# Optimization experiments

Hardware: AMD Instinct MI355X
Metric: run time of the kernel (lower is better)

The kernel has to match this reference:

```python
import jax, jax.numpy as jnp
import numpy as np

S = 1024   # qlen = klen (mems=None)
B = 4
D = 1024   # d_model
N = 16     # n_head
H = 64     # d_head
R = 2 * S  # relative position embedding length = klen + qlen
EPS = 1e-12
SCALE = float(1.0 / np.sqrt(H))


def setup_inputs() -> dict:
    key = jax.random.key(0)
    ks = jax.random.split(key, 14)
    h = jax.random.normal(ks[0], (S, B, D), dtype=jnp.float32)
    r = jax.random.normal(ks[1], (R, B, D), dtype=jnp.float32)
    # segment ids -> one-hot same/diff segment matrix [i, j, b, 2]
    seg_ids = jax.random.randint(ks[2], (S, B), 0, 2)
    diff = (seg_ids[:, None, :] != seg_ids[None, :, :]).astype(jnp.int32)  # [S,S,B]
    seg_mat = jax.nn.one_hot(diff, 2, dtype=jnp.float32)  # [S,S,B,2]
    # causal attention mask: 1 where key position j > query position i
    causal = (jnp.arange(S)[None, :] > jnp.arange(S)[:, None]).astype(jnp.float32)
    attn_mask = jnp.broadcast_to(causal[:, :, None, None], (S, S, B, 1))
    w = lambda k, shape: 0.02 * jax.random.normal(k, shape, dtype=jnp.float32)
    return {
        "h": h, "r": r, "seg_mat": seg_mat, "attn_mask": attn_mask,
        "Wq": w(ks[3], (D, N, H)), "Wk": w(ks[4], (D, N, H)),
        "Wv": w(ks[5], (D, N, H)), "Wo": w(ks[6], (D, N, H)),
        "Wr": w(ks[7], (D, N, H)),
        "r_w_bias": w(ks[8], (N, H)), "r_r_bias": w(ks[9], (N, H)),
        "r_s_bias": w(ks[10], (N, H)), "seg_embed": w(ks[11], (2, N, H)),
        "ln_scale": jnp.ones((D,), jnp.float32), "ln_bias": jnp.zeros((D,), jnp.float32),
    }


def rel_shift_bnij(x, klen):
    # x: [b, n, i, j_r] with j_r = klen + qlen
    b, n, i, j = x.shape
    x = x.reshape(b, n, j, i)[:, :, 1:, :].reshape(b, n, i, j - 1)
    return x[:, :, :, :klen]


def layer_norm(x, scale, bias):
    mu = jnp.mean(x, axis=-1, keepdims=True)
    var = jnp.mean(jnp.square(x - mu), axis=-1, keepdims=True)
    return (x - mu) * jax.lax.rsqrt(var + EPS) * scale + bias


def reference(h, r, seg_mat, attn_mask, Wq, Wk, Wv, Wo, Wr,
              r_w_bias, r_r_bias, r_s_bias, seg_embed, ln_scale, ln_bias):
    # projections (mems=None => cat = h)
    q_head = jnp.einsum('ibh,hnd->ibnd', h, Wq)
    k_head_h = jnp.einsum('ibh,hnd->ibnd', h, Wk)
    v_head_h = jnp.einsum('ibh,hnd->ibnd', h, Wv)
    k_head_r = jnp.einsum('ibh,hnd->ibnd', r, Wr)

    klen = k_head_h.shape[0]
    # content-based score
    ac = jnp.einsum('ibnd,jbnd->bnij', q_head + r_w_bias, k_head_h)
    # position-based score with relative shift
    bd = jnp.einsum('ibnd,jbnd->bnij', q_head + r_r_bias, k_head_r)
    bd = rel_shift_bnij(bd, klen)
    # segment-based score
    ef = jnp.einsum('ibnd,snd->ibns', q_head + r_s_bias, seg_embed)
    ef = jnp.einsum('ijbs,ibns->bnij', seg_mat, ef)

    attn_score = (ac + bd + ef) * SCALE
    attn_score = attn_score - 1e30 * jnp.transpose(attn_mask, (2, 3, 0, 1))  # ijbn->bnij
    attn_prob = jax.nn.softmax(attn_score, axis=3)

    attn_vec = jnp.einsum('bnij,jbnd->ibnd', attn_prob, v_head_h)
    attn_out = jnp.einsum('ibnd,hnd->ibh', attn_vec, Wo) + h  # residual
    return layer_norm(attn_out, ln_scale, ln_bias)
```

## Files before the change

### kernel.cpp

```cpp
#include <hip/hip_runtime.h>

#define Sq 1024
#define Bb 4
#define Dm 1024
#define Nh 16
#define Hd 64

typedef unsigned short ushort_t;
typedef __attribute__((ext_vector_type(8))) short s8v;
typedef __attribute__((ext_vector_type(8))) unsigned short us8;
typedef __attribute__((ext_vector_type(4))) float f32x4;
typedef __attribute__((ext_vector_type(2))) __fp16 fp16x2;

__device__ __forceinline__ float bf2f(ushort_t u) {
  union { unsigned int i; float f; } t; t.i = ((unsigned int)u) << 16; return t.f;
}
__device__ __forceinline__ ushort_t f2bf(float f) {
  union { float f; unsigned int i; } t; t.f = f;
  unsigned int lsb = (t.i >> 16) & 1u;
  t.i += 0x7fffu + lsb;
  return (ushort_t)(t.i >> 16);
}

__device__ __forceinline__ void load4(const float* p, float* o) {
  const float4 v = *(const float4*)p;
  o[0] = v.x; o[1] = v.y; o[2] = v.z; o[3] = v.w;
}

__device__ __forceinline__ float wave_reduce_sum(float v) {
#pragma unroll
  for (int off = 32; off; off >>= 1) v += __shfl_xor(v, off, 64);
  return v;
}

__device__ __forceinline__ void gl_lds16(const ushort_t* g, ushort_t* l) {
  __builtin_amdgcn_global_load_lds(
      (const __attribute__((address_space(1))) unsigned int*)g,
      (__attribute__((address_space(3))) unsigned int*)l, 16, 0, 0);
}

template <int MODE>
__device__ __forceinline__ void gemm128(const ushort_t* __restrict__ A,
                                        const ushort_t* __restrict__ B,
                                        void* __restrict__ Cv,
                                        const float* __restrict__ bias0,
                                        int bm, int bn) {
  __shared__ ushort_t As[128 * 32];
  __shared__ ushort_t Bs[128 * 32];
  const int tid = threadIdx.x;
  const int w = tid >> 6, lane = tid & 63;
  const int quad = lane >> 4, l16 = lane & 15;
  const int wm = (w & 1) * 64, wn = (w >> 1) * 64;
  const int srow0 = 32 * w + (lane >> 2);
  const int scb = (lane & 3) * 16;
  f32x4 acc[4][4] = {};

  for (int k0 = 0; k0 < 1024; k0 += 32) {
    __syncthreads();
#pragma unroll
    for (int c = 0; c < 2; ++c) {
      const int row = srow0 + c * 16;
      const int cbs = scb ^ (((row >> 1) & 3) << 4);
      gl_lds16(A + (size_t)(bm + row) * 1024 + k0 + (cbs >> 1),
               &As[(32 * w + c * 16) * 32]);
      gl_lds16(B + (size_t)(bn + row) * 1024 + k0 + (cbs >> 1),
               &Bs[(32 * w + c * 16) * 32]);
    }
    __syncthreads();
    s8v av[4], bv[4];
    const int sw = ((l16 >> 1) & 3) << 4;
    const int cbb = ((quad * 16) ^ sw) >> 1;
#pragma unroll
    for (int i = 0; i < 4; ++i) {
      av[i] = *(const s8v*)&As[(wm + i * 16 + l16) * 32 + cbb];
      bv[i] = *(const s8v*)&Bs[(wn + i * 16 + l16) * 32 + cbb];
    }
#pragma unroll
    for (int i = 0; i < 4; ++i)
#pragma unroll
      for (int j = 0; j < 4; ++j)
        acc[i][j] = __builtin_amdgcn_mfma_f32_16x16x32_bf16(av[i], bv[j], acc[i][j], 0, 0, 0);
  }

  float bj[4];
  if (MODE == 3) {
#pragma unroll
    for (int j = 0; j < 4; ++j) bj[j] = bias0[bn + wn + j * 16 + l16];
  }
#pragma unroll
  for (int i = 0; i < 4; ++i) {
#pragma unroll
    for (int j = 0; j < 4; ++j) {
      const int cg = bn + wn + j * 16 + l16;
#pragma unroll
      for (int reg = 0; reg < 4; ++reg) {
        const int mg = bm + wm + i * 16 + quad * 4 + reg;
        const float v = acc[i][j][reg];
        if (MODE == 3) {
          ((ushort_t*)Cv)[((size_t)(cg >> 6) * 1024 + mg) * 64 + (cg & 63)] =
              f2bf((v + bj[j]) * 0.125f);
        } else if (MODE == 0) {
          ((ushort_t*)Cv)[((size_t)(cg >> 6) * 1024 + mg) * 64 + (cg & 63)] = f2bf(v);
        } else {
          ((float*)Cv)[(size_t)mg * 1024 + cg] = v;
        }
      }
    }
  }
}

__global__ __launch_bounds__(256) void conv_hr(const float* __restrict__ h,
                                               const float* __restrict__ r,
                                               const float* __restrict__ Wo,
                                               ushort_t* __restrict__ h_bf,
                                               ushort_t* __restrict__ r_bf,
                                               ushort_t* __restrict__ Wo_bf) {
  const int i = blockIdx.x, b = blockIdx.y;
  const int d0 = threadIdx.x * 4;
  {
    const float4 v = *(const float4*)&h[(size_t)(i * 4 + b) * 1024 + d0];
    ushort4 o; o.x = f2bf(v.x); o.y = f2bf(v.y); o.z = f2bf(v.z); o.w = f2bf(v.w);
    *(ushort4*)&h_bf[(size_t)b * 1048576 + (size_t)i * 1024 + d0] = o;
  }
  {
    const float4 v = *(const float4*)&r[(size_t)(i * 4 + 4 + b) * 1024 + d0];
    ushort4 o; o.x = f2bf(v.x); o.y = f2bf(v.y); o.z = f2bf(v.z); o.w = f2bf(v.w);
    *(ushort4*)&r_bf[(size_t)b * 1048576 + (size_t)i * 1024 + d0] = o;
  }
  if (b == 0) {
    const float4 v = *(const float4*)&Wo[(size_t)i * 1024 + d0];
    ushort4 o; o.x = f2bf(v.x); o.y = f2bf(v.y); o.z = f2bf(v.z); o.w = f2bf(v.w);
    *(ushort4*)&Wo_bf[(size_t)i * 1024 + d0] = o;
  }
}

__global__ __launch_bounds__(256) void conv_wt(const float* __restrict__ Wq,
                                               const float* __restrict__ Wk,
                                               const float* __restrict__ Wv,
                                               const float* __restrict__ Wr,
                                               ushort_t* __restrict__ Wt) {
  const int z = blockIdx.z;
  const float* W = (z == 0) ? Wq : (z == 1) ? Wk : (z == 2) ? Wv : Wr;
  ushort_t* O = Wt + (size_t)z * 1048576;
  __shared__ float t[64][68];
  const int n0 = blockIdx.x * 64, k0 = blockIdx.y * 64;
  const int tr = threadIdx.x >> 4, tc = (threadIdx.x & 15) * 4;
#pragma unroll
  for (int rr = 0; rr < 4; ++rr) {
    const int r_ = tr + rr * 16;
    const float4 v = *(const float4*)&W[(size_t)(k0 + r_) * 1024 + n0 + tc];
    t[r_][tc] = v.x; t[r_][tc + 1] = v.y; t[r_][tc + 2] = v.z; t[r_][tc + 3] = v.w;
  }
  __syncthreads();
#pragma unroll
  for (int rr = 0; rr < 4; ++rr) {
    const int nr = tr + rr * 16;
    ushort4 o;
    o.x = f2bf(t[tc + 0][nr]); o.y = f2bf(t[tc + 1][nr]);
    o.z = f2bf(t[tc + 2][nr]); o.w = f2bf(t[tc + 3][nr]);
    *(ushort4*)&O[(size_t)(n0 + nr) * 1024 + k0 + tc] = o;
  }
}

__global__ __launch_bounds__(256) void sseg_kernel(const float* __restrict__ seg_mat,
                                                   const float* __restrict__ rwb,
                                                   const float* __restrict__ rrb,
                                                   float* __restrict__ sseg,
                                                   float* __restrict__ drr) {
  const int idx = blockIdx.x * 256 + threadIdx.x;
  const int b = idx >> 10, j = idx & 1023;
  sseg[b * 1024 + j] = seg_mat[(size_t)j * 8 + b * 2 + 1];
  if (idx < 1024) drr[idx] = (rrb[idx] - rwb[idx]) * 0.125f;
}

__global__ __launch_bounds__(256) void projA(
    const ushort_t* __restrict__ h_bf, const ushort_t* __restrict__ r_bf,
    const ushort_t* __restrict__ Wt, const float* __restrict__ rwb,
    ushort_t* __restrict__ qcS, ushort_t* __restrict__ KSl,
    ushort_t* __restrict__ KRS) {
  const int z = blockIdx.z, zi = z % 3, b = z / 3;
  const int zz = (zi == 2) ? 3 : zi;
  const size_t slab = (size_t)Nh * Sq * Hd;
  const ushort_t* A = (zz == 3 ? r_bf : h_bf) + (size_t)b * 1048576;
  const ushort_t* B = Wt + (size_t)zz * 1048576;
  const int bm = blockIdx.y * 128, bn = blockIdx.x * 128;
  if (zi == 0) gemm128<3>(A, B, qcS + b * slab, rwb, bm, bn);
  else if (zi == 1) gemm128<0>(A, B, KSl + b * slab, nullptr, bm, bn);
  else gemm128<0>(A, B, KRS + b * slab, nullptr, bm, bn);
}

__global__ __launch_bounds__(256) void projV(const ushort_t* __restrict__ h_bf,
                                             const ushort_t* __restrict__ Wt,
                                             ushort_t* __restrict__ VS) {
  const int b = blockIdx.z;
  const size_t slab = (size_t)Nh * Sq * Hd;
  gemm128<0>(h_bf + (size_t)b * 1048576, Wt + (size_t)2 * 1048576, VS + b * slab,
             nullptr, blockIdx.y * 128, blockIdx.x * 128);
}

__global__ __launch_bounds__(256) void vtrans(const ushort_t* __restrict__ VS,
                                              ushort_t* __restrict__ VTP) {
  const int j0 = blockIdx.x * 64, n = blockIdx.y, b = blockIdx.z;
  const size_t slab = (size_t)Nh * Sq * Hd;
  const ushort_t* src = VS + b * slab + (size_t)n * Sq * Hd;
  ushort_t* dst = VTP + b * slab + (size_t)n * Hd * Sq;
  __shared__ ushort_t t[64][72];
  const int tid = threadIdx.x;
#pragma unroll
  for (int it = 0; it < 2; ++it) {
    const int row = it * 32 + (tid >> 3);
    const int c = (tid & 7) * 8;
    const us8 v = *(const us8*)&src[(size_t)(j0 + row) * 64 + c];
#pragma unroll
    for (int e = 0; e < 8; ++e) t[row][c + e] = v[e];
  }
  __syncthreads();
#pragma unroll
  for (int it = 0; it < 2; ++it) {
    const int idx = it * 256 + tid;
    const int d = idx >> 3;
    const int kc = (idx & 7) * 8;
    us8 o;
#pragma unroll
    for (int e = 0; e < 8; ++e) {
      const int k = kc + e;
      o[e] = t[(k & 3) * 16 + (k >> 2)][d];
    }
    *(us8*)&dst[(size_t)d * Sq + j0 + kc] = o;
  }
}

__global__ __launch_bounds__(256) void attn_mfma(
    const ushort_t* __restrict__ QCS, const ushort_t* __restrict__ KS,
    const ushort_t* __restrict__ VTS, const ushort_t* __restrict__ KRS,
    const float* __restrict__ rwb, const float* __restrict__ rsb,
    const float* __restrict__ seg_embed, const float* __restrict__ sseg,
    const float* __restrict__ drr, ushort_t* __restrict__ AVbf) {
  const int nb = blockIdx.x;
  const int n = nb & 15, b = nb >> 4;
  const int i0b = (int)(gridDim.y - 1 - blockIdx.y) * 32;
  const int tid = threadIdx.x;
  const int w = tid >> 6, lane = tid & 63;
  const int quad = lane >> 4, l16 = lane & 15;
  const int ht = w >> 1;
  const int jp = w & 1;
  const int i0s = i0b + ht * 16;
  const size_t slab = (size_t)Nh * Sq * Hd;
  const size_t nS = (size_t)n * Sq;
  const ushort_t* Qh = QCS + b * slab + nS * Hd;
  const ushort_t* Kh = KS + b * slab + nS * Hd;
  const ushort_t* Vh = VTS + b * slab + (size_t)n * Hd * Sq;
  const ushort_t* KRh = KRS + b * slab + nS * Hd;
  const float* ssegb = sseg + b * Sq;

  __shared__ ushort_t P_s[4][16 * 64];
  __shared__ float o_s[2][2][16][66];
  __shared__ float l_s[2][2][16];

  s8v qc[2], qr[2];
  float efa_v, efb_v;
  {
    const int qrow = i0s + l16;
    const size_t qbase = (size_t)qrow * 64;
    float p0 = 0.f, p1 = 0.f;
#pragma unroll
    for (int ks = 0; ks < 2; ++ks) {
      const int dl = ks * 32 + quad * 8;
      const int db = n * 64 + dl;
      const s8v qv = *(const s8v*)&Qh[qbase + dl];
      qc[ks] = qv;
      float dr8[8], w8[8], s8a[8], e08[8], e18[8];
      load4(drr + db, dr8); load4(drr + db + 4, dr8 + 4);
      load4(rwb + db, w8);  load4(rwb + db + 4, w8 + 4);
      load4(rsb + db, s8a); load4(rsb + db + 4, s8a + 4);
      load4(seg_embed + db, e08); load4(seg_embed + db + 4, e08 + 4);
      load4(seg_embed + Nh * 64 + db, e18); load4(seg_embed + Nh * 64 + db + 4, e18 + 4);
#pragma unroll
      for (int e = 0; e < 8; ++e) {
        const float qcf = bf2f((ushort_t)qv[e]);
        qr[ks][e] = (short)f2bf(qcf + dr8[e]);
        const float qs = qcf * 8.f - w8[e] + s8a[e];
        p0 += qs * e08[e];
        p1 += qs * e18[e];
      }
    }
    p0 += __shfl_xor(p0, 16, 64); p0 += __shfl_xor(p0, 32, 64);
    p1 += __shfl_xor(p1, 16, 64); p1 += __shfl_xor(p1, 32, 64);
    const float si = ssegb[qrow];
    const float de = p1 - p0;
    efa_v = (p0 + de * si) * 0.125f;
    efb_v = de * (1.f - 2.f * si) * 0.125f;
  }

  float efa_r[4], efb_r[4];
  int bp_idx[4], selhi[4];
#pragma unroll
  for (int reg = 0; reg < 4; ++reg) {
    const int il = quad * 4 + reg;
    efa_r[reg] = __shfl(efa_v, il, 64);
    efb_r[reg] = __shfl(efb_v, il, 64);
    const int off = l16 + 15 - il;
    bp_idx[reg] = (((quad << 4) | (off & 15)) << 2);
    selhi[reg] = off >> 4;
  }

  f32x4 o[4] = {};
  float l_r[4] = {0.f, 0.f, 0.f, 0.f};
  char* Pb = (char*)P_s[w];

  const int n_jt = i0s / 64 + 1;
  for (int jt = jp; jt < n_jt; jt += 2) {
    const int j0 = jt * 64;
    const bool last = (jt == n_jt - 1);

    f32x4 sc[4];
    const ushort_t* Kt = Kh + (size_t)j0 * 64;
#pragma unroll
    for (int u = 0; u < 4; ++u) {
      const int ro = (u * 16 + l16) * 64 + quad * 8;
      f32x4 a = {};
      a = __builtin_amdgcn_mfma_f32_16x16x32_bf16(qc[0], *(const s8v*)&Kt[ro], a, 0, 0, 0);
      a = __builtin_amdgcn_mfma_f32_16x16x32_bf16(qc[1], *(const s8v*)&Kt[ro + 32], a, 0, 0, 0);
      sc[u] = a;
    }

    f32x4 bdw[5];
    const ushort_t* KRt = KRh + (size_t)(1008 + j0 - i0s) * 64;
    const int rlim = 15 + (i0s & 63);
#pragma unroll
    for (int u = 0; u < 5; ++u) {
      int rr = u * 16 + l16;
      if (last && rr > rlim) rr = rlim;
      const int ro = rr * 64 + quad * 8;
      f32x4 a = {};
      a = __builtin_amdgcn_mfma_f32_16x16x32_bf16(qr[0], *(const s8v*)&KRt[ro], a, 0, 0, 0);
      a = __builtin_amdgcn_mfma_f32_16x16x32_bf16(qr[1], *(const s8v*)&KRt[ro + 32], a, 0, 0, 0);
      bdw[u] = a;
    }

    int pk[4][4];
#pragma unroll
    for (int u = 0; u < 4; ++u)
#pragma unroll
      for (int reg = 0; reg < 4; ++reg) {
        const fp16x2 t = __builtin_amdgcn_cvt_pkrtz(bdw[u][reg], bdw[u + 1][reg]);
        pk[u][reg] = __builtin_bit_cast(int, t);
      }

    float sj[4];
#pragma unroll
    for (int u = 0; u < 4; ++u) sj[u] = ssegb[j0 + u * 16 + l16];
    float p[4][4];
#pragma unroll
    for (int u = 0; u < 4; ++u) {
#pragma unroll
      for (int reg = 0; reg < 4; ++reg) {
        const int g = __builtin_amdgcn_ds_bpermute(bp_idx[reg], pk[u][reg]);
        const __fp16 hf =
            __builtin_bit_cast(__fp16, (unsigned short)(selhi[reg] ? (g >> 16) : g));
        p[u][reg] = __expf(sc[u][reg] + (float)hf + efa_r[reg] + efb_r[reg] * sj[u]);
      }
    }
    if (last) {
#pragma unroll
      for (int u = 0; u < 4; ++u)
#pragma unroll
        for (int reg = 0; reg < 4; ++reg)
          if (j0 + u * 16 + l16 > i0s + quad * 4 + reg) p[u][reg] = 0.f;
    }
#pragma unroll
    for (int reg = 0; reg < 4; ++reg)
      l_r[reg] += p[0][reg] + p[1][reg] + p[2][reg] + p[3][reg];

#pragma unroll
    for (int reg = 0; reg < 4; ++reg) {
      const int i = quad * 4 + reg;
      const unsigned int lo = (unsigned int)f2bf(p[0][reg]) | ((unsigned int)f2bf(p[1][reg]) << 16);
      const unsigned int hi = (unsigned int)f2bf(p[2][reg]) | ((unsigned int)f2bf(p[3][reg]) << 16);
      *(uint2*)(Pb + i * 128 + ((((l16 >> 1) ^ (i & 7)) << 4) | ((l16 & 1) << 3))) =
          make_uint2(lo, hi);
    }
    s8v pa[2];
#pragma unroll
    for (int ks = 0; ks < 2; ++ks)
      pa[ks] = *(const s8v*)(Pb + l16 * 128 + (((ks * 4 + quad) ^ (l16 & 7)) << 4));

    const ushort_t* Vt = Vh + j0;
#pragma unroll
    for (int u = 0; u < 4; ++u) {
      const size_t vro = (size_t)(u * 16 + l16) * Sq + quad * 8;
      o[u] = __builtin_amdgcn_mfma_f32_16x16x32_bf16(pa[0], *(const s8v*)&Vt[vro], o[u], 0, 0, 0);
      o[u] = __builtin_amdgcn_mfma_f32_16x16x32_bf16(pa[1], *(const s8v*)&Vt[vro + 32], o[u], 0, 0, 0);
    }
  }

#pragma unroll
  for (int reg = 0; reg < 4; ++reg) {
#pragma unroll
    for (int off = 1; off < 16; off <<= 1) l_r[reg] += __shfl_xor(l_r[reg], off, 64);
  }
  if (l16 == 0) {
#pragma unroll
    for (int reg = 0; reg < 4; ++reg) l_s[ht][jp][quad * 4 + reg] = l_r[reg];
  }
#pragma unroll
  for (int u = 0; u < 4; ++u)
#pragma unroll
    for (int reg = 0; reg < 4; ++reg)
      o_s[ht][jp][quad * 4 + reg][u * 16 + l16] = o[u][reg];
  __syncthreads();

  {
    const int mht = tid >> 7;
    const int rem = tid & 127;
    const int row = rem >> 3;
    const int c0 = (rem & 7) * 8;
    const float lt = l_s[mht][0][row] + l_s[mht][1][row];
    const float inv = 1.0f / lt;
    us8 ob;
#pragma unroll
    for (int e = 0; e < 8; ++e)
      ob[e] = f2bf((o_s[mht][0][row][c0 + e] + o_s[mht][1][row][c0 + e]) * inv);
    *(us8*)&AVbf[((size_t)(i0b + mht * 16 + row) * Bb + b) * 1024 + n * 64 + c0] = ob;
  }
}

__global__ __launch_bounds__(256) void ln_res(float* __restrict__ out,
                                              const float* __restrict__ h,
                                              const float* __restrict__ scale,
                                              const float* __restrict__ bias) {
  const int row = blockIdx.x;
  const int tid = threadIdx.x;
  __shared__ float red1[4], red2[4];
  float v[4];
  float sum = 0.f;
#pragma unroll
  for (int c = 0; c < 4; ++c) {
    const int idx = tid + c * 256;
    const float x = out[(size_t)row * Dm + idx] + h[(size_t)row * Dm + idx];
    v[c] = x;
    sum += x;
  }
  sum = wave_reduce_sum(sum);
  const int wid = tid >> 6, lane = tid & 63;
  if (!lane) red1[wid] = sum;
  __syncthreads();
  const float mean = (red1[0] + red1[1] + red1[2] + red1[3]) * (1.0f / 1024.0f);
  float sq = 0.f;
#pragma unroll
  for (int c = 0; c < 4; ++c) {
    const float t = v[c] - mean;
    sq += t * t;
  }
  sq = wave_reduce_sum(sq);
  if (!lane) red2[wid] = sq;
  __syncthreads();
  const float var = (red2[0] + red2[1] + red2[2] + red2[3]) * (1.0f / 1024.0f);
  const float rstd = rsqrtf(var + 1e-12f);
#pragma unroll
  for (int c = 0; c < 4; ++c) {
    const int idx = tid + c * 256;
    out[(size_t)row * Dm + idx] = (v[c] - mean) * rstd * scale[idx] + bias[idx];
  }
}

__global__ __launch_bounds__(256) void outproj128(const ushort_t* __restrict__ AV,
                                                  const ushort_t* __restrict__ Wo,
                                                  float* __restrict__ AO) {
  gemm128<1>(AV, Wo, AO, nullptr, blockIdx.y * 128, blockIdx.x * 128);
}

extern "C" void kernel_launch(void* const* d_in, const int* in_sizes, int n_in,
                              void* d_out, int out_size, void* d_ws, size_t ws_size,
                              hipStream_t stream) {
  const float* h = (const float*)d_in[0];
  const float* r = (const float*)d_in[1];
  const float* seg_mat = (const float*)d_in[2];
  const float* Wq = (const float*)d_in[4];
  const float* Wk = (const float*)d_in[5];
  const float* Wv = (const float*)d_in[6];
  const float* Wo = (const float*)d_in[7];
  const float* Wr = (const float*)d_in[8];
  const float* rwb = (const float*)d_in[9];
  const float* rrb = (const float*)d_in[10];
  const float* rsb = (const float*)d_in[11];
  const float* seg_embed = (const float*)d_in[12];
  const float* ln_scale = (const float*)d_in[13];
  const float* ln_bias = (const float*)d_in[14];

  char* wsb = (char*)d_ws;
  const size_t MB = 1024 * 1024;
  const size_t slabsz = (size_t)Nh * Sq * Hd;
  ushort_t* h_bf = (ushort_t*)(wsb + 0);
  ushort_t* r_bf = (ushort_t*)(wsb + 8 * MB);
  ushort_t* Wt = (ushort_t*)(wsb + 16 * MB);
  ushort_t* Wo_bf = (ushort_t*)(wsb + 24 * MB);
  ushort_t* qcS = (ushort_t*)(wsb + 26 * MB);
  ushort_t* KSl = (ushort_t*)(wsb + 34 * MB);
  ushort_t* VTP = (ushort_t*)(wsb + 42 * MB);
  ushort_t* KRS = (ushort_t*)(wsb + 50 * MB);
  float* sseg = (float*)(wsb + 58 * MB);
  float* drr = (float*)(wsb + 58 * MB + 16 * 1024);
  ushort_t* VS = r_bf;
  ushort_t* AVbf = h_bf;
  float* out = (float*)d_out;

  conv_hr<<<dim3(1024, 4), 256, 0, stream>>>(h, r, Wo, h_bf, r_bf, Wo_bf);
  conv_wt<<<dim3(16, 16, 4), 256, 0, stream>>>(Wq, Wk, Wv, Wr, Wt);
  sseg_kernel<<<16, 256, 0, stream>>>(seg_mat, rwb, rrb, sseg, drr);
  projA<<<dim3(8, 8, 12), 256, 0, stream>>>(h_bf, r_bf, Wt, rwb, qcS, KSl, KRS);
  projV<<<dim3(8, 8, 4), 256, 0, stream>>>(h_bf, Wt, VS);
  vtrans<<<dim3(16, 16, 4), 256, 0, stream>>>(VS, VTP);
  attn_mfma<<<dim3(64, 32), 256, 0, stream>>>(qcS, KSl, VTP, KRS, rwb, rsb,
                                              seg_embed, sseg, drr, AVbf);
  outproj128<<<dim3(8, 32), 256, 0, stream>>>(AVbf, Wo_bf, out);
  ln_res<<<4096, 256, 0, stream>>>(out, h, ln_scale, ln_bias);
}
```

Baseline: 380.8 us.

## Merge prep kernels, fuse V projection, and give each attention wave two query tiles

The three conversion and prep kernels become a single launch, and the V projection joins the Q/K/R projection launch, which removes launch overhead and lets the projections fill the GPU together. V is now staged in the output buffer because r_bf is read in the same launch. The attention kernel drops to 128 threads, with each wave handling 32 query rows as two 16-row subtiles. This reuses the K, V and shared relative-position K loads across both subtiles, at the cost of more registers per wave and fewer waves per block.

```diff
diff --git a/kernel.cpp b/kernel.cpp
--- a/kernel.cpp
+++ b/kernel.cpp
@@ -109,93 +109,78 @@
   }
 }
 
-__global__ __launch_bounds__(256) void conv_hr(const float* __restrict__ h,
-                                               const float* __restrict__ r,
-                                               const float* __restrict__ Wo,
-                                               ushort_t* __restrict__ h_bf,
-                                               ushort_t* __restrict__ r_bf,
-                                               ushort_t* __restrict__ Wo_bf) {
-  const int i = blockIdx.x, b = blockIdx.y;
-  const int d0 = threadIdx.x * 4;
-  {
-    const float4 v = *(const float4*)&h[(size_t)(i * 4 + b) * 1024 + d0];
-    ushort4 o; o.x = f2bf(v.x); o.y = f2bf(v.y); o.z = f2bf(v.z); o.w = f2bf(v.w);
-    *(ushort4*)&h_bf[(size_t)b * 1048576 + (size_t)i * 1024 + d0] = o;
-  }
-  {
-    const float4 v = *(const float4*)&r[(size_t)(i * 4 + 4 + b) * 1024 + d0];
-    ushort4 o; o.x = f2bf(v.x); o.y = f2bf(v.y); o.z = f2bf(v.z); o.w = f2bf(v.w);
-    *(ushort4*)&r_bf[(size_t)b * 1048576 + (size_t)i * 1024 + d0] = o;
-  }
-  if (b == 0) {
-    const float4 v = *(const float4*)&Wo[(size_t)i * 1024 + d0];
-    ushort4 o; o.x = f2bf(v.x); o.y = f2bf(v.y); o.z = f2bf(v.z); o.w = f2bf(v.w);
-    *(ushort4*)&Wo_bf[(size_t)i * 1024 + d0] = o;
-  }
-}
-
-__global__ __launch_bounds__(256) void conv_wt(const float* __restrict__ Wq,
-                                               const float* __restrict__ Wk,
-                                               const float* __restrict__ Wv,
-                                               const float* __restrict__ Wr,
-                                               ushort_t* __restrict__ Wt) {
-  const int z = blockIdx.z;
-  const float* W = (z == 0) ? Wq : (z == 1) ? Wk : (z == 2) ? Wv : Wr;
-  ushort_t* O = Wt + (size_t)z * 1048576;
+__global__ __launch_bounds__(256) void prep(
+    const float* __restrict__ h, const float* __restrict__ r,
+    const float* __restrict__ Wq, const float* __restrict__ Wk,
+    const float* __restrict__ Wv, const float* __restrict__ Wr,
+    const float* __restrict__ Wo, const float* __restrict__ seg_mat,
+    const float* __restrict__ rwb, const float* __restrict__ rrb,
+    ushort_t* __restrict__ h_bf, ushort_t* __restrict__ r_bf,
+    ushort_t* __restrict__ Wt, ushort_t* __restrict__ Wo_bf,
+    float* __restrict__ sseg, float* __restrict__ drr) {
   __shared__ float t[64][68];
-  const int n0 = blockIdx.x * 64, k0 = blockIdx.y * 64;
-  const int tr = threadIdx.x >> 4, tc = (threadIdx.x & 15) * 4;
-#pragma unroll
-  for (int rr = 0; rr < 4; ++rr) {
-    const int r_ = tr + rr * 16;
-    const float4 v = *(const float4*)&W[(size_t)(k0 + r_) * 1024 + n0 + tc];
-    t[r_][tc] = v.x; t[r_][tc + 1] = v.y; t[r_][tc + 2] = v.z; t[r_][tc + 3] = v.w;
-  }
-  __syncthreads();
-#pragma unroll
-  for (int rr = 0; rr < 4; ++rr) {
-    const int nr = tr + rr * 16;
-    ushort4 o;
-    o.x = f2bf(t[tc + 0][nr]); o.y = f2bf(t[tc + 1][nr]);
-    o.z = f2bf(t[tc + 2][nr]); o.w = f2bf(t[tc + 3][nr]);
-    *(ushort4*)&O[(size_t)(n0 + nr) * 1024 + k0 + tc] = o;
-  }
-}
-
-__global__ __launch_bounds__(256) void sseg_kernel(const float* __restrict__ seg_mat,
-                                                   const float* __restrict__ rwb,
-                                                   const float* __restrict__ rrb,
-                                                   float* __restrict__ sseg,
-                                                   float* __restrict__ drr) {
-  const int idx = blockIdx.x * 256 + threadIdx.x;
-  const int b = idx >> 10, j = idx & 1023;
-  sseg[b * 1024 + j] = seg_mat[(size_t)j * 8 + b * 2 + 1];
-  if (idx < 1024) drr[idx] = (rrb[idx] - rwb[idx]) * 0.125f;
-}
-
-__global__ __launch_bounds__(256) void projA(
+  const int x = blockIdx.x, y = blockIdx.y, tid = threadIdx.x;
+  if (y < 4) {
+    const int b = y, i = x, d0 = tid * 4;
+    {
+      const float4 v = *(const float4*)&h[(size_t)(i * 4 + b) * 1024 + d0];
+      ushort4 o; o.x = f2bf(v.x); o.y = f2bf(v.y); o.z = f2bf(v.z); o.w = f2bf(v.w);
+      *(ushort4*)&h_bf[(size_t)b * 1048576 + (size_t)i * 1024 + d0] = o;
+    }
+    {
+      const float4 v = *(const float4*)&r[(size_t)(i * 4 + 4 + b) * 1024 + d0];
+      ushort4 o; o.x = f2bf(v.x); o.y = f2bf(v.y); o.z = f2bf(v.z); o.w = f2bf(v.w);
+      *(ushort4*)&r_bf[(size_t)b * 1048576 + (size_t)i * 1024 + d0] = o;
+    }
+    if (b == 0) {
+      const float4 v = *(const float4*)&Wo[(size_t)i * 1024 + d0];
+      ushort4 o; o.x = f2bf(v.x); o.y = f2bf(v.y); o.z = f2bf(v.z); o.w = f2bf(v.w);
+      *(ushort4*)&Wo_bf[(size_t)i * 1024 + d0] = o;
+      if (x < 16) {
+        const int idx = x * 256 + tid;
+        const int bb = idx >> 10, j = idx & 1023;
+        sseg[bb * 1024 + j] = seg_mat[(size_t)j * 8 + bb * 2 + 1];
+        if (idx < 1024) drr[idx] = (rrb[idx] - rwb[idx]) * 0.125f;
+      }
+    }
+  } else {
+    const int z = x >> 8, sub = x & 255;
+    const float* W = (z == 0) ? Wq : (z == 1) ? Wk : (z == 2) ? Wv : Wr;
+    ushort_t* O = Wt + (size_t)z * 1048576;
+    const int n0 = (sub & 15) * 64, k0 = (sub >> 4) * 64;
+    const int tr = tid >> 4, tc = (tid & 15) * 4;
+#pragma unroll
+    for (int rr = 0; rr < 4; ++rr) {
+      const int r_ = tr + rr * 16;
+      const float4 v = *(const float4*)&W[(size_t)(k0 + r_) * 1024 + n0 + tc];
+      t[r_][tc] = v.x; t[r_][tc + 1] = v.y; t[r_][tc + 2] = v.z; t[r_][tc + 3] = v.w;
+    }
+    __syncthreads();
+#pragma unroll
+    for (int rr = 0; rr < 4; ++rr) {
+      const int nr = tr + rr * 16;
+      ushort4 o;
+      o.x = f2bf(t[tc + 0][nr]); o.y = f2bf(t[tc + 1][nr]);
+      o.z = f2bf(t[tc + 2][nr]); o.w = f2bf(t[tc + 3][nr]);
+      *(ushort4*)&O[(size_t)(n0 + nr) * 1024 + k0 + tc] = o;
+    }
+  }
+}
+
+__global__ __launch_bounds__(256) void projAV(
     const ushort_t* __restrict__ h_bf, const ushort_t* __restrict__ r_bf,
     const ushort_t* __restrict__ Wt, const float* __restrict__ rwb,
     ushort_t* __restrict__ qcS, ushort_t* __restrict__ KSl,
-    ushort_t* __restrict__ KRS) {
-  const int z = blockIdx.z, zi = z % 3, b = z / 3;
-  const int zz = (zi == 2) ? 3 : zi;
+    ushort_t* __restrict__ KRS, ushort_t* __restrict__ VS) {
+  const int z = blockIdx.z, zz = z & 3, b = z >> 2;
   const size_t slab = (size_t)Nh * Sq * Hd;
   const ushort_t* A = (zz == 3 ? r_bf : h_bf) + (size_t)b * 1048576;
   const ushort_t* B = Wt + (size_t)zz * 1048576;
   const int bm = blockIdx.y * 128, bn = blockIdx.x * 128;
-  if (zi == 0) gemm128<3>(A, B, qcS + b * slab, rwb, bm, bn);
-  else if (zi == 1) gemm128<0>(A, B, KSl + b * slab, nullptr, bm, bn);
+  if (zz == 0) gemm128<3>(A, B, qcS + b * slab, rwb, bm, bn);
+  else if (zz == 1) gemm128<0>(A, B, KSl + b * slab, nullptr, bm, bn);
+  else if (zz == 2) gemm128<0>(A, B, VS + b * slab, nullptr, bm, bn);
   else gemm128<0>(A, B, KRS + b * slab, nullptr, bm, bn);
-}
-
-__global__ __launch_bounds__(256) void projV(const ushort_t* __restrict__ h_bf,
-                                             const ushort_t* __restrict__ Wt,
-                                             ushort_t* __restrict__ VS) {
-  const int b = blockIdx.z;
-  const size_t slab = (size_t)Nh * Sq * Hd;
-  gemm128<0>(h_bf + (size_t)b * 1048576, Wt + (size_t)2 * 1048576, VS + b * slab,
-             nullptr, blockIdx.y * 128, blockIdx.x * 128);
 }
 
 __global__ __launch_bounds__(256) void vtrans(const ushort_t* __restrict__ VS,
@@ -230,7 +215,7 @@
   }
 }
 
-__global__ __launch_bounds__(256) void attn_mfma(
+__global__ __launch_bounds__(128) void attn_mfma(
     const ushort_t* __restrict__ QCS, const ushort_t* __restrict__ KS,
     const ushort_t* __restrict__ VTS, const ushort_t* __restrict__ KRS,
     const float* __restrict__ rwb, const float* __restrict__ rsb,
@@ -240,11 +225,9 @@
   const int n = nb & 15, b = nb >> 4;
   const int i0b = (int)(gridDim.y - 1 - blockIdx.y) * 32;
   const int tid = threadIdx.x;
-  const int w = tid >> 6, lane = tid & 63;
+  const int w = tid >> 6;
+  const int lane = tid & 63;
   const int quad = lane >> 4, l16 = lane & 15;
-  const int ht = w >> 1;
-  const int jp = w & 1;
-  const int i0s = i0b + ht * 16;
   const size_t slab = (size_t)Nh * Sq * Hd;
   const size_t nS = (size_t)n * Sq;
   const ushort_t* Qh = QCS + b * slab + nS * Hd;
@@ -253,22 +236,18 @@
   const ushort_t* KRh = KRS + b * slab + nS * Hd;
   const float* ssegb = sseg + b * Sq;
 
-  __shared__ ushort_t P_s[4][16 * 64];
-  __shared__ float o_s[2][2][16][66];
-  __shared__ float l_s[2][2][16];
-
-  s8v qc[2], qr[2];
-  float efa_v, efb_v;
+  __shared__ ushort_t P_s[2][32 * 64];
+  __shared__ float o_s[2][32][66];
+  __shared__ float l_s[2][32];
+
+  s8v qc[2][2], qr[2][2];
+  float efa_v[2], efb_v[2];
   {
-    const int qrow = i0s + l16;
-    const size_t qbase = (size_t)qrow * 64;
-    float p0 = 0.f, p1 = 0.f;
+    float p0[2] = {0.f, 0.f}, p1[2] = {0.f, 0.f};
 #pragma unroll
     for (int ks = 0; ks < 2; ++ks) {
       const int dl = ks * 32 + quad * 8;
       const int db = n * 64 + dl;
-      const s8v qv = *(const s8v*)&Qh[qbase + dl];
-      qc[ks] = qv;
       float dr8[8], w8[8], s8a[8], e08[8], e18[8];
       load4(drr + db, dr8); load4(drr + db + 4, dr8 + 4);
       load4(rwb + db, w8);  load4(rwb + db + 4, w8 + 4);
@@ -276,152 +255,196 @@
       load4(seg_embed + db, e08); load4(seg_embed + db + 4, e08 + 4);
       load4(seg_embed + Nh * 64 + db, e18); load4(seg_embed + Nh * 64 + db + 4, e18 + 4);
 #pragma unroll
-      for (int e = 0; e < 8; ++e) {
-        const float qcf = bf2f((ushort_t)qv[e]);
-        qr[ks][e] = (short)f2bf(qcf + dr8[e]);
-        const float qs = qcf * 8.f - w8[e] + s8a[e];
-        p0 += qs * e08[e];
-        p1 += qs * e18[e];
-      }
-    }
-    p0 += __shfl_xor(p0, 16, 64); p0 += __shfl_xor(p0, 32, 64);
-    p1 += __shfl_xor(p1, 16, 64); p1 += __shfl_xor(p1, 32, 64);
-    const float si = ssegb[qrow];
-    const float de = p1 - p0;
-    efa_v = (p0 + de * si) * 0.125f;
-    efb_v = de * (1.f - 2.f * si) * 0.125f;
-  }
-
-  float efa_r[4], efb_r[4];
+      for (int sub = 0; sub < 2; ++sub) {
+        const s8v qv = *(const s8v*)&Qh[(size_t)(i0b + sub * 16 + l16) * 64 + dl];
+        qc[sub][ks] = qv;
+#pragma unroll
+        for (int e = 0; e < 8; ++e) {
+          const float qcf = bf2f((ushort_t)qv[e]);
+          qr[sub][ks][e] = (short)f2bf(qcf + dr8[e]);
+          const float qs = qcf * 8.f - w8[e] + s8a[e];
+          p0[sub] += qs * e08[e];
+          p1[sub] += qs * e18[e];
+        }
+      }
+    }
+#pragma unroll
+    for (int sub = 0; sub < 2; ++sub) {
+      p0[sub] += __shfl_xor(p0[sub], 16, 64); p0[sub] += __shfl_xor(p0[sub], 32, 64);
+      p1[sub] += __shfl_xor(p1[sub], 16, 64); p1[sub] += __shfl_xor(p1[sub], 32, 64);
+      const float si = ssegb[i0b + sub * 16 + l16];
+      const float de = p1[sub] - p0[sub];
+      efa_v[sub] = (p0[sub] + de * si) * 0.125f;
+      efb_v[sub] = de * (1.f - 2.f * si) * 0.125f;
+    }
+  }
+
+  float efa_r[2][4], efb_r[2][4];
   int bp_idx[4], selhi[4];
 #pragma unroll
   for (int reg = 0; reg < 4; ++reg) {
     const int il = quad * 4 + reg;
-    efa_r[reg] = __shfl(efa_v, il, 64);
-    efb_r[reg] = __shfl(efb_v, il, 64);
+#pragma unroll
+    for (int sub = 0; sub < 2; ++sub) {
+      efa_r[sub][reg] = __shfl(efa_v[sub], il, 64);
+      efb_r[sub][reg] = __shfl(efb_v[sub], il, 64);
+    }
     const int off = l16 + 15 - il;
     bp_idx[reg] = (((quad << 4) | (off & 15)) << 2);
     selhi[reg] = off >> 4;
   }
 
-  f32x4 o[4] = {};
-  float l_r[4] = {0.f, 0.f, 0.f, 0.f};
+  f32x4 o[2][4] = {};
+  float l_r[2][4] = {};
   char* Pb = (char*)P_s[w];
 
-  const int n_jt = i0s / 64 + 1;
-  for (int jt = jp; jt < n_jt; jt += 2) {
+  const int n_jt = i0b / 64 + 1;
+  for (int jt = w; jt < n_jt; jt += 2) {
     const int j0 = jt * 64;
     const bool last = (jt == n_jt - 1);
 
-    f32x4 sc[4];
+    f32x4 sc[2][4];
     const ushort_t* Kt = Kh + (size_t)j0 * 64;
 #pragma unroll
     for (int u = 0; u < 4; ++u) {
       const int ro = (u * 16 + l16) * 64 + quad * 8;
-      f32x4 a = {};
-      a = __builtin_amdgcn_mfma_f32_16x16x32_bf16(qc[0], *(const s8v*)&Kt[ro], a, 0, 0, 0);
-      a = __builtin_amdgcn_mfma_f32_16x16x32_bf16(qc[1], *(const s8v*)&Kt[ro + 32], a, 0, 0, 0);
-      sc[u] = a;
-    }
-
-    f32x4 bdw[5];
-    const ushort_t* KRt = KRh + (size_t)(1008 + j0 - i0s) * 64;
-    const int rlim = 15 + (i0s & 63);
-#pragma unroll
-    for (int u = 0; u < 5; ++u) {
-      int rr = u * 16 + l16;
-      if (last && rr > rlim) rr = rlim;
-      const int ro = rr * 64 + quad * 8;
-      f32x4 a = {};
-      a = __builtin_amdgcn_mfma_f32_16x16x32_bf16(qr[0], *(const s8v*)&KRt[ro], a, 0, 0, 0);
-      a = __builtin_amdgcn_mfma_f32_16x16x32_bf16(qr[1], *(const s8v*)&KRt[ro + 32], a, 0, 0, 0);
-      bdw[u] = a;
-    }
-
-    int pk[4][4];
-#pragma unroll
-    for (int u = 0; u < 4; ++u)
+      const s8v k0v = *(const s8v*)&Kt[ro];
+      const s8v k1v = *(const s8v*)&Kt[ro + 32];
+#pragma unroll
+      for (int sub = 0; sub < 2; ++sub) {
+        f32x4 a = {};
+        a = __builtin_amdgcn_mfma_f32_16x16x32_bf16(qc[sub][0], k0v, a, 0, 0, 0);
+        a = __builtin_amdgcn_mfma_f32_16x16x32_bf16(qc[sub][1], k1v, a, 0, 0, 0);
+        sc[sub][u] = a;
+      }
+    }
+
+    f32x4 bdw[2][5];
+    const int base1 = 992 + j0 - i0b;
+#pragma unroll
+    for (int f = 0; f < 6; ++f) {
+      int g = base1 + f * 16 + l16;
+      if (g > 1023) g = 1023;
+      const int ro = g * 64 + quad * 8;
+      const s8v r0v = *(const s8v*)&KRh[ro];
+      const s8v r1v = *(const s8v*)&KRh[ro + 32];
+      if (f < 5) {
+        f32x4 a = {};
+        a = __builtin_amdgcn_mfma_f32_16x16x32_bf16(qr[1][0], r0v, a, 0, 0, 0);
+        a = __builtin_amdgcn_mfma_f32_16x16x32_bf16(qr[1][1], r1v, a, 0, 0, 0);
+        bdw[1][f] = a;
+      }
+      if (f >= 1) {
+        f32x4 a = {};
+        a = __builtin_amdgcn_mfma_f32_16x16x32_bf16(qr[0][0], r0v, a, 0, 0, 0);
+        a = __builtin_amdgcn_mfma_f32_16x16x32_bf16(qr[0][1], r1v, a, 0, 0, 0);
+        bdw[0][f - 1] = a;
+      }
+    }
+
+    float sj[4];
+#pragma unroll
+    for (int u = 0; u < 4; ++u) sj[u] = ssegb[j0 + u * 16 + l16];
+#pragma unroll
+    for (int sub = 0; sub < 2; ++sub) {
+      float p[4][4];
+#pragma unroll
+      for (int u = 0; u < 4; ++u) {
+#pragma unroll
+        for (int reg = 0; reg < 4; ++reg) {
+          const fp16x2 t = __builtin_amdgcn_cvt_pkrtz(bdw[sub][u][reg], bdw[sub][u + 1][reg]);
+          const int g = __builtin_amdgcn_ds_bpermute(bp_idx[reg], __builtin_bit_cast(int, t));
+          const __fp16 hf =
+              __builtin_bit_cast(__fp16, (unsigned short)(selhi[reg] ? (g >> 16) : g));
+          p[u][reg] = __expf(sc[sub][u][reg] + (float)hf + efa_r[sub][reg] +
+                             efb_r[sub][reg] * sj[u]);
+        }
+      }
+      if (last) {
+#pragma unroll
+        for (int u = 0; u < 4; ++u)
+#pragma unroll
+          for (int reg = 0; reg < 4; ++reg)
+            if (j0 + u * 16 + l16 > i0b + sub * 16 + quad * 4 + reg) p[u][reg] = 0.f;
+      }
+#pragma unroll
+      for (int reg = 0; reg < 4; ++reg)
+        l_r[sub][reg] += p[0][reg] + p[1][reg] + p[2][reg] + p[3][reg];
+
 #pragma unroll
       for (int reg = 0; reg < 4; ++reg) {
-        const fp16x2 t = __builtin_amdgcn_cvt_pkrtz(bdw[u][reg], bdw[u + 1][reg]);
-        pk[u][reg] = __builtin_bit_cast(int, t);
-      }
-
-    float sj[4];
-#pragma unroll
-    for (int u = 0; u < 4; ++u) sj[u] = ssegb[j0 + u * 16 + l16];
-    float p[4][4];
-#pragma unroll
-    for (int u = 0; u < 4; ++u) {
-#pragma unroll
-      for (int reg = 0; reg < 4; ++reg) {
-        const int g = __builtin_amdgcn_ds_bpermute(bp_idx[reg], pk[u][reg]);
-        const __fp16 hf =
-            __builtin_bit_cast(__fp16, (unsigned short)(selhi[reg] ? (g >> 16) : g));
-        p[u][reg] = __expf(sc[u][reg] + (float)hf + efa_r[reg] + efb_r[reg] * sj[u]);
-      }
-    }
-    if (last) {
-#pragma unroll
-      for (int u = 0; u < 4; ++u)
-#pragma unroll
-        for (int reg = 0; reg < 4; ++reg)
-          if (j0 + u * 16 + l16 > i0s + quad * 4 + reg) p[u][reg] = 0.f;
-    }
-#pragma unroll
-    for (int reg = 0; reg < 4; ++reg)
-      l_r[reg] += p[0][reg] + p[1][reg] + p[2][reg] + p[3][reg];
-
-#pragma unroll
-    for (int reg = 0; reg < 4; ++reg) {
-      const int i = quad * 4 + reg;
-      const unsigned int lo = (unsigned int)f2bf(p[0][reg]) | ((unsigned int)f2bf(p[1][reg]) << 16);
-      const unsigned int hi = (unsigned int)f2bf(p[2][reg]) | ((unsigned int)f2bf(p[3][reg]) << 16);
-      *(uint2*)(Pb + i * 128 + ((((l16 >> 1) ^ (i & 7)) << 4) | ((l16 & 1) << 3))) =
-          make_uint2(lo, hi);
-    }
-    s8v pa[2];
-#pragma unroll
-    for (int ks = 0; ks < 2; ++ks)
-      pa[ks] = *(const s8v*)(Pb + l16 * 128 + (((ks * 4 + quad) ^ (l16 & 7)) << 4));
+        const int i = sub * 16 + quad * 4 + reg;
+        const unsigned int lo =
+            (unsigned int)f2bf(p[0][reg]) | ((unsigned int)f2bf(p[1][reg]) << 16);
+        const unsigned int hi =
+            (unsigned int)f2bf(p[2][reg]) | ((unsigned int)f2bf(p[3][reg]) << 16);
+        *(uint2*)(Pb + i * 128 + ((((l16 >> 1) ^ (i & 7)) << 4) | ((l16 & 1) << 3))) =
+            make_uint2(lo, hi);
+      }
+    }
+
+    s8v pa[2][2];
+#pragma unroll
+    for (int sub = 0; sub < 2; ++sub)
+#pragma unroll
+      for (int ks = 0; ks < 2; ++ks)
+        pa[sub][ks] = *(const s8v*)(Pb + (sub * 16 + l16) * 128 +
+                                    (((ks * 4 + quad) ^ (l16 & 7)) << 4));
 
     const ushort_t* Vt = Vh + j0;
 #pragma unroll
     for (int u = 0; u < 4; ++u) {
       const size_t vro = (size_t)(u * 16 + l16) * Sq + quad * 8;
-      o[u] = __builtin_amdgcn_mfma_f32_16x16x32_bf16(pa[0], *(const s8v*)&Vt[vro], o[u], 0, 0, 0);
-      o[u] = __builtin_amdgcn_mfma_f32_16x16x32_bf16(pa[1], *(const s8v*)&Vt[vro + 32], o[u], 0, 0, 0);
-    }
-  }
-
-#pragma unroll
-  for (int reg = 0; reg < 4; ++reg) {
-#pragma unroll
-    for (int off = 1; off < 16; off <<= 1) l_r[reg] += __shfl_xor(l_r[reg], off, 64);
-  }
+      const s8v v0 = *(const s8v*)&Vt[vro];
+      const s8v v1 = *(const s8v*)&Vt[vro + 32];
+#pragma unroll
+      for (int sub = 0; sub < 2; ++sub) {
+        o[sub][u] = __builtin_amdgcn_mfma_f32_16x16x32_bf16(pa[sub][0], v0, o[sub][u], 0, 0, 0);
+        o[sub][u] = __builtin_amdgcn_mfma_f32_16x16x32_bf16(pa[sub][1], v1, o[sub][u], 0, 0, 0);
+      }
+    }
+  }
+
+#pragma unroll
+  for (int sub = 0; sub < 2; ++sub)
+#pragma unroll
+    for (int reg = 0; reg < 4; ++reg) {
+#pragma unroll
+      for (int off = 1; off < 16; off <<= 1)
+        l_r[sub][reg] += __shfl_xor(l_r[sub][reg], off, 64);
+    }
   if (l16 == 0) {
 #pragma unroll
-    for (int reg = 0; reg < 4; ++reg) l_s[ht][jp][quad * 4 + reg] = l_r[reg];
-  }
-#pragma unroll
-  for (int u = 0; u < 4; ++u)
-#pragma unroll
-    for (int reg = 0; reg < 4; ++reg)
-      o_s[ht][jp][quad * 4 + reg][u * 16 + l16] = o[u][reg];
+    for (int sub = 0; sub < 2; ++sub)
+#pragma unroll
+      for (int reg = 0; reg < 4; ++reg)
+        l_s[w][sub * 16 + quad * 4 + reg] = l_r[sub][reg];
+  }
+#pragma unroll
+  for (int sub = 0; sub < 2; ++sub)
+#pragma unroll
+    for (int u = 0; u < 4; ++u)
+#pragma unroll
+      for (int reg = 0; reg < 4; ++reg)
+        o_s[w][sub * 16 + quad * 4 + reg][u * 16 + l16] = o[sub][u][reg];
   __syncthreads();
 
   {
-    const int mht = tid >> 7;
-    const int rem = tid & 127;
-    const int row = rem >> 3;
-    const int c0 = (rem & 7) * 8;
-    const float lt = l_s[mht][0][row] + l_s[mht][1][row];
+    const int row = tid >> 2;
+    const int c0 = (tid & 3) * 16;
+    const float lt = l_s[0][row] + l_s[1][row];
     const float inv = 1.0f / lt;
-    us8 ob;
-#pragma unroll
-    for (int e = 0; e < 8; ++e)
-      ob[e] = f2bf((o_s[mht][0][row][c0 + e] + o_s[mht][1][row][c0 + e]) * inv);
-    *(us8*)&AVbf[((size_t)(i0b + mht * 16 + row) * Bb + b) * 1024 + n * 64 + c0] = ob;
+    const size_t base = ((size_t)(i0b + row) * Bb + b) * 1024 + n * 64;
+#pragma unroll
+    for (int half = 0; half < 2; ++half) {
+      us8 ob;
+#pragma unroll
+      for (int e = 0; e < 8; ++e) {
+        const int c = c0 + half * 8 + e;
+        ob[e] = f2bf((o_s[0][row][c] + o_s[1][row][c]) * inv);
+      }
+      *(us8*)&AVbf[base + c0 + half * 8] = ob;
+    }
   }
 }
 
@@ -501,17 +524,16 @@
   ushort_t* KRS = (ushort_t*)(wsb + 50 * MB);
   float* sseg = (float*)(wsb + 58 * MB);
   float* drr = (float*)(wsb + 58 * MB + 16 * 1024);
-  ushort_t* VS = r_bf;
+  ushort_t* VS = (ushort_t*)d_out;
   ushort_t* AVbf = h_bf;
   float* out = (float*)d_out;
-
-  conv_hr<<<dim3(1024, 4), 256, 0, stream>>>(h, r, Wo, h_bf, r_bf, Wo_bf);
-  conv_wt<<<dim3(16, 16, 4), 256, 0, stream>>>(Wq, Wk, Wv, Wr, Wt);
-  sseg_kernel<<<16, 256, 0, stream>>>(seg_mat, rwb, rrb, sseg, drr);
-  projA<<<dim3(8, 8, 12), 256, 0, stream>>>(h_bf, r_bf, Wt, rwb, qcS, KSl, KRS);
-  projV<<<dim3(8, 8, 4), 256, 0, stream>>>(h_bf, Wt, VS);
+  (void)slabsz;
+
+  prep<<<dim3(1024, 5), 256, 0, stream>>>(h, r, Wq, Wk, Wv, Wr, Wo, seg_mat,
+                                          rwb, rrb, h_bf, r_bf, Wt, Wo_bf, sseg, drr);
+  projAV<<<dim3(8, 8, 16), 256, 0, stream>>>(h_bf, r_bf, Wt, rwb, qcS, KSl, KRS, VS);
   vtrans<<<dim3(16, 16, 4), 256, 0, stream>>>(VS, VTP);
-  attn_mfma<<<dim3(64, 32), 256, 0, stream>>>(qcS, KSl, VTP, KRS, rwb, rsb,
+  attn_mfma<<<dim3(64, 32), 128, 0, stream>>>(qcS, KSl, VTP, KRS, rwb, rsb,
                                               seg_embed, sseg, drr, AVbf);
   outproj128<<<dim3(8, 32), 256, 0, stream>>>(AVbf, Wo_bf, out);
   ln_res<<<4096, 256, 0, stream>>>(out, h, ln_scale, ln_bias);
```

Result: faster. 324.3 us (-14.8%).
